# Performance work log

Measured on AMD Instinct MI355X. Metric: run time of the kernel, lower is better.

Reference implementation:

```python
import jax, jax.numpy as jnp
import numpy as np

N = 40000      # nodes
E = 20000      # hyperedges
M = 640000     # incidences
D = 128        # num_features == num_classes == MLP_hidden
ALPHA = 0.1
EPS = 1e-5


def _layernorm(h, g, b):
    mu = jnp.mean(h, axis=-1, keepdims=True)
    var = jnp.mean((h - mu) ** 2, axis=-1, keepdims=True)
    return (h - mu) * jax.lax.rsqrt(var + EPS) * g + b


def _mlp(x, w1, b1, g, be, w2, b2):
    h = x @ w1 + b1
    h = jax.nn.relu(_layernorm(h, g, be))
    return h @ w2 + b2


def _scatter_mean(vals, idx, num_segments):
    s = jax.ops.segment_sum(vals, idx, num_segments=num_segments)
    cnt = jax.ops.segment_sum(jnp.ones((vals.shape[0],), vals.dtype), idx,
                              num_segments=num_segments)
    return s / jnp.maximum(cnt, 1.0)[:, None]


def setup_inputs() -> dict:
    key = jax.random.key(0)
    ks = jax.random.split(key, 16)
    x = jax.random.normal(ks[0], (N, D), dtype=jnp.float32)
    vertex = jax.random.randint(ks[1], (M,), 0, N)
    edges = jax.random.randint(ks[2], (M,), 0, E)
    edge_index = jnp.stack([vertex, edges]).astype(jnp.int64)

    def lin(k, fin, fout):
        s = 1.0 / np.sqrt(fin)
        kw, kb = jax.random.split(k)
        return (jax.random.uniform(kw, (fin, fout), jnp.float32, -s, s),
                jax.random.uniform(kb, (fout,), jnp.float32, -s, s))

    w1_1, b1_1 = lin(ks[3], D, D)
    w1_2, b1_2 = lin(ks[4], D, D)
    w2_1, b2_1 = lin(ks[5], 2 * D, D)
    w2_2, b2_2 = lin(ks[6], D, D)
    g1 = jnp.ones((D,), jnp.float32)
    be1 = jnp.zeros((D,), jnp.float32)
    g2 = jnp.ones((D,), jnp.float32)
    be2 = jnp.zeros((D,), jnp.float32)
    return {"x": x, "w1_1": w1_1, "b1_1": b1_1, "g1": g1, "be1": be1,
            "w1_2": w1_2, "b1_2": b1_2, "w2_1": w2_1, "b2_1": b2_1,
            "g2": g2, "be2": be2, "w2_2": w2_2, "b2_2": b2_2,
            "edge_index": edge_index}


def reference(x, w1_1, b1_1, g1, be1, w1_2, b1_2,
              w2_1, b2_1, g2, be2, w2_2, b2_2, edge_index):
    vertex = edge_index[0]
    edges = edge_index[1]
    X0 = x
    # gather -> MLP1 -> scatter-mean onto hyperedges
    Xve = _mlp(x[vertex], w1_1, b1_1, g1, be1, w1_2, b1_2)   # [M, D]
    Xe = _scatter_mean(Xve, edges, E)                         # [E, D]
    # gather back -> concat -> MLP2 -> scatter-mean onto nodes
    Xev = Xe[edges]                                           # [M, D]
    Xev = _mlp(jnp.concatenate([x[vertex], Xev], axis=-1),
               w2_1, b2_1, g2, be2, w2_2, b2_2)               # [M, D]
    Xv = _scatter_mean(Xev, vertex, N)                        # [N, D]
    return (1.0 - ALPHA) * Xv + ALPHA * X0
```

## Files before the change

### kernel.cpp

```cpp
#include <hip/hip_runtime.h>

#define DF 128
constexpr int NN = 40000;
constexpr int EE = 20000;
constexpr int MM = 640000;
constexpr float EPSF = 1e-5f;
constexpr float ALPHA = 0.1f;
constexpr int SE = 88;
constexpr int SV = 56;

constexpr int NB_BUILD = MM / 256;
constexpr int NB_GEMM  = (NN + 63) / 64;
constexpr int NB_COMBO = (128 * 128 + 128 + 255) / 256;

template <int EPI, bool STATS>
__device__ __forceinline__ void gemm_tile(const float* __restrict__ A, int nrows,
                                          const float* __restrict__ W,
                                          const float* __restrict__ bias,
                                          const float* __restrict__ bias2,
                                          const int* __restrict__ cnt,
                                          const float* __restrict__ g,
                                          const float* __restrict__ be,
                                          const float* __restrict__ xres,
                                          float* __restrict__ C,
                                          float* __restrict__ sOut,
                                          float* __restrict__ qOut,
                                          int blk, float* as) {
  int tid = threadIdx.x;
  int rbase = blk * 64;

  #pragma unroll
  for (int j = 0; j < 8; ++j) {
    int q = tid + j * 256;
    int row = q >> 5;
    int c4 = q & 31;
    int grow = rbase + row;
    float4 v = make_float4(0.f, 0.f, 0.f, 0.f);
    if (grow < nrows) {
      v = *reinterpret_cast<const float4*>(A + (size_t)grow * DF + c4 * 4);
    }
    *reinterpret_cast<float4*>(&as[row * 132 + c4 * 4]) = v;
  }
  __syncthreads();

  int tc = tid & 15;
  int tr = tid >> 4;
  int cbase = tc * 8;

  float acc[4][8];
  #pragma unroll
  for (int i = 0; i < 4; ++i)
    #pragma unroll
    for (int c = 0; c < 8; ++c) acc[i][c] = 0.0f;

  #pragma unroll 4
  for (int k = 0; k < 128; ++k) {
    float w[8];
    *reinterpret_cast<float4*>(&w[0]) = *reinterpret_cast<const float4*>(W + k * DF + cbase);
    *reinterpret_cast<float4*>(&w[4]) = *reinterpret_cast<const float4*>(W + k * DF + cbase + 4);
    float a[4];
    #pragma unroll
    for (int i = 0; i < 4; ++i) a[i] = as[(tr * 4 + i) * 132 + k];
    #pragma unroll
    for (int i = 0; i < 4; ++i)
      #pragma unroll
      for (int c = 0; c < 8; ++c) acc[i][c] += a[i] * w[c];
  }

  float bv[8];
  #pragma unroll
  for (int c = 0; c < 8; ++c) bv[c] = 0.0f;
  if (bias) {
    #pragma unroll
    for (int c = 0; c < 8; ++c) bv[c] = bias[cbase + c];
  }
  if (bias2) {
    #pragma unroll
    for (int c = 0; c < 8; ++c) bv[c] += bias2[cbase + c];
  }
  #pragma unroll
  for (int i = 0; i < 4; ++i)
    #pragma unroll
    for (int c = 0; c < 8; ++c) acc[i][c] += bv[c];

  if (STATS) {
    #pragma unroll
    for (int i = 0; i < 4; ++i) {
      float s = 0.f, q = 0.f;
      #pragma unroll
      for (int c = 0; c < 8; ++c) { s += acc[i][c]; q += acc[i][c] * acc[i][c]; }
      #pragma unroll
      for (int mask = 1; mask <= 8; mask <<= 1) {
        s += __shfl_xor(s, mask, 16);
        q += __shfl_xor(q, mask, 16);
      }
      if (tc == 0) {
        int grow = rbase + tr * 4 + i;
        if (grow < nrows) { sOut[grow] = s; qOut[grow] = q; }
      }
    }
  }

  if (EPI == 1) {
    float gv[8], bev[8];
    #pragma unroll
    for (int c = 0; c < 8; ++c) { gv[c] = g[cbase + c]; bev[c] = be[cbase + c]; }
    #pragma unroll
    for (int i = 0; i < 4; ++i) {
      float s = 0.f, s2 = 0.f;
      #pragma unroll
      for (int c = 0; c < 8; ++c) { s += acc[i][c]; s2 += acc[i][c] * acc[i][c]; }
      #pragma unroll
      for (int mask = 1; mask <= 8; mask <<= 1) {
        s += __shfl_xor(s, mask, 16);
        s2 += __shfl_xor(s2, mask, 16);
      }
      float mean = s * (1.0f / 128.0f);
      float var = s2 * (1.0f / 128.0f) - mean * mean;
      float rs = rsqrtf(var + EPSF);
      #pragma unroll
      for (int c = 0; c < 8; ++c) {
        float y = (acc[i][c] - mean) * rs * gv[c] + bev[c];
        acc[i][c] = fmaxf(y, 0.0f);
      }
    }
  }

  #pragma unroll
  for (int i = 0; i < 4; ++i) {
    int grow = rbase + tr * 4 + i;
    if (grow >= nrows) continue;
    float outv[8];
    if (EPI == 2) {
      int cv = cnt[grow];
      #pragma unroll
      for (int c = 0; c < 8; ++c) {
        float xv = xres[(size_t)grow * DF + cbase + c];
        outv[c] = (cv == 0) ? ALPHA * xv : (1.0f - ALPHA) * acc[i][c] + ALPHA * xv;
      }
    } else {
      #pragma unroll
      for (int c = 0; c < 8; ++c) outv[c] = acc[i][c];
    }
    *reinterpret_cast<float4*>(C + (size_t)grow * DF + cbase) =
        make_float4(outv[0], outv[1], outv[2], outv[3]);
    *reinterpret_cast<float4*>(C + (size_t)grow * DF + cbase + 4) =
        make_float4(outv[4], outv[5], outv[6], outv[7]);
  }
}

__global__ __launch_bounds__(256) void fusedA(
    const int* __restrict__ ei,
    int* __restrict__ cnt_e, int* __restrict__ cnt_v,
    ushort* __restrict__ lst_e, ushort* __restrict__ lst_v,
    const float* __restrict__ x,
    const float* __restrict__ w1_1, const float* __restrict__ b1_1,
    const float* __restrict__ g1, const float* __restrict__ be1,
    const float* __restrict__ w2_1,
    const float* __restrict__ w1_2, const float* __restrict__ b1_2,
    float* __restrict__ H1, float* __restrict__ A2,
    float* __restrict__ sA, float* __restrict__ qA,
    float* __restrict__ Wc, float* __restrict__ bc) {
  __shared__ float as[64 * 132];
  int blk = blockIdx.x;
  if (blk < NB_BUILD) {
    int m = blk * 256 + threadIdx.x;
    int v = ei[m];
    int e = ei[MM + m];
    int pe = atomicAdd(&cnt_e[e], 1);
    lst_e[e * SE + pe] = (ushort)v;
    int pv = atomicAdd(&cnt_v[v], 1);
    lst_v[v * SV + pv] = (ushort)e;
  } else if (blk < NB_BUILD + NB_GEMM) {
    gemm_tile<1, false>(x, NN, w1_1, b1_1, nullptr, nullptr, g1, be1, nullptr,
                        H1, nullptr, nullptr, blk - NB_BUILD, as);
  } else if (blk < NB_BUILD + 2 * NB_GEMM) {
    gemm_tile<0, true>(x, NN, w2_1, nullptr, nullptr, nullptr, nullptr, nullptr,
                       nullptr, A2, sA, qA, blk - NB_BUILD - NB_GEMM, as);
  } else {
    const float* w2b = w2_1 + 128 * DF;
    int out = (blk - NB_BUILD - 2 * NB_GEMM) * 256 + threadIdx.x;
    if (out < 16384) {
      int i = out >> 7;
      int j = out & 127;
      float s = 0.0f;
      for (int k = 0; k < 128; ++k) s += w1_2[i * DF + k] * w2b[k * DF + j];
      Wc[out] = s;
    } else if (out < 16512) {
      int j = out - 16384;
      float s = 0.0f;
      for (int k = 0; k < 128; ++k) s += b1_2[k] * w2b[k * DF + j];
      bc[j] = s;
    }
  }
}

template <int EPI, bool STATS>
__global__ __launch_bounds__(256) void gemm128(const float* __restrict__ A, int nrows,
                                               const float* __restrict__ W,
                                               const float* __restrict__ bias,
                                               const float* __restrict__ bias2,
                                               const int* __restrict__ cnt,
                                               const float* __restrict__ g,
                                               const float* __restrict__ be,
                                               const float* __restrict__ xres,
                                               float* __restrict__ C,
                                               float* __restrict__ sOut,
                                               float* __restrict__ qOut) {
  __shared__ float as[64 * 132];
  gemm_tile<EPI, STATS>(A, nrows, W, bias, bias2, cnt, g, be, xres, C, sOut,
                        qOut, blockIdx.x, as);
}

__global__ __launch_bounds__(256) void gather1(const float* __restrict__ H1,
                                               const int* __restrict__ cnt_e,
                                               const ushort* __restrict__ lst_e,
                                               float* __restrict__ Hemean) {
  int e = blockIdx.x * 4 + (threadIdx.x >> 6);
  int lane = threadIdx.x & 63;
  int g = lane >> 4;
  int l = lane & 15;
  int deg = cnt_e[e];
  const ushort* lst = lst_e + e * SE;
  float4 acc0 = make_float4(0.f, 0.f, 0.f, 0.f);
  float4 acc1 = make_float4(0.f, 0.f, 0.f, 0.f);
  for (int i = g; i < deg; i += 4) {
    int v = lst[i];
    const float* src = H1 + (size_t)v * DF + l * 8;
    float4 h0 = *reinterpret_cast<const float4*>(src);
    float4 h1 = *reinterpret_cast<const float4*>(src + 4);
    acc0.x += h0.x; acc0.y += h0.y; acc0.z += h0.z; acc0.w += h0.w;
    acc1.x += h1.x; acc1.y += h1.y; acc1.z += h1.z; acc1.w += h1.w;
  }
  #pragma unroll
  for (int mask = 16; mask <= 32; mask <<= 1) {
    acc0.x += __shfl_xor(acc0.x, mask); acc0.y += __shfl_xor(acc0.y, mask);
    acc0.z += __shfl_xor(acc0.z, mask); acc0.w += __shfl_xor(acc0.w, mask);
    acc1.x += __shfl_xor(acc1.x, mask); acc1.y += __shfl_xor(acc1.y, mask);
    acc1.z += __shfl_xor(acc1.z, mask); acc1.w += __shfl_xor(acc1.w, mask);
  }
  if (g == 0) {
    float sc = 1.0f / (float)(deg > 1 ? deg : 1);
    float* dst = Hemean + (size_t)e * DF + l * 8;
    *reinterpret_cast<float4*>(dst) =
        make_float4(acc0.x * sc, acc0.y * sc, acc0.z * sc, acc0.w * sc);
    *reinterpret_cast<float4*>(dst + 4) =
        make_float4(acc1.x * sc, acc1.y * sc, acc1.z * sc, acc1.w * sc);
  }
}

__global__ __launch_bounds__(256) void gather2(const float* __restrict__ A2,
                                               const float* __restrict__ B,
                                               const float* __restrict__ sA,
                                               const float* __restrict__ qA,
                                               const float* __restrict__ sB,
                                               const float* __restrict__ qB,
                                               const int* __restrict__ cnt_v,
                                               const ushort* __restrict__ lst_v,
                                               const float* __restrict__ g2,
                                               const float* __restrict__ be2,
                                               float* __restrict__ Svmean) {
  int v = blockIdx.x * 4 + (threadIdx.x >> 6);
  int lane = threadIdx.x & 63;
  int g = lane >> 4;
  int l = lane & 15;
  const float* ap = A2 + (size_t)v * DF + l * 8;
  float4 a0 = *reinterpret_cast<const float4*>(ap);
  float4 a1 = *reinterpret_cast<const float4*>(ap + 4);
  float4 gv0 = *reinterpret_cast<const float4*>(g2 + l * 8);
  float4 gv1 = *reinterpret_cast<const float4*>(g2 + l * 8 + 4);
  float4 bv0 = *reinterpret_cast<const float4*>(be2 + l * 8);
  float4 bv1 = *reinterpret_cast<const float4*>(be2 + l * 8 + 4);
  float sAv = sA[v];
  float qAv = qA[v];
  int deg = cnt_v[v];
  const ushort* lst = lst_v + v * SV;
  float4 acc0 = make_float4(0.f, 0.f, 0.f, 0.f);
  float4 acc1 = make_float4(0.f, 0.f, 0.f, 0.f);
  for (int i = g; i < deg; i += 4) {
    int e = lst[i];
    const float* bp = B + (size_t)e * DF + l * 8;
    float4 b0 = *reinterpret_cast<const float4*>(bp);
    float4 b1 = *reinterpret_cast<const float4*>(bp + 4);
    float d = a0.x * b0.x + a0.y * b0.y + a0.z * b0.z + a0.w * b0.w +
              a1.x * b1.x + a1.y * b1.y + a1.z * b1.z + a1.w * b1.w;
    d += __shfl_xor(d, 1, 16);
    d += __shfl_xor(d, 2, 16);
    d += __shfl_xor(d, 4, 16);
    d += __shfl_xor(d, 8, 16);
    float s = sAv + sB[e];
    float q = qAv + qB[e] + 2.0f * d;
    float mean = s * (1.0f / 128.0f);
    float var = q * (1.0f / 128.0f) - mean * mean;
    float rs = rsqrtf(var + EPSF);
    float mrs = mean * rs;
    float t;
    t = (a0.x + b0.x) * rs - mrs; acc0.x += fmaxf(t * gv0.x + bv0.x, 0.f);
    t = (a0.y + b0.y) * rs - mrs; acc0.y += fmaxf(t * gv0.y + bv0.y, 0.f);
    t = (a0.z + b0.z) * rs - mrs; acc0.z += fmaxf(t * gv0.z + bv0.z, 0.f);
    t = (a0.w + b0.w) * rs - mrs; acc0.w += fmaxf(t * gv0.w + bv0.w, 0.f);
    t = (a1.x + b1.x) * rs - mrs; acc1.x += fmaxf(t * gv1.x + bv1.x, 0.f);
    t = (a1.y + b1.y) * rs - mrs; acc1.y += fmaxf(t * gv1.y + bv1.y, 0.f);
    t = (a1.z + b1.z) * rs - mrs; acc1.z += fmaxf(t * gv1.z + bv1.z, 0.f);
    t = (a1.w + b1.w) * rs - mrs; acc1.w += fmaxf(t * gv1.w + bv1.w, 0.f);
  }
  #pragma unroll
  for (int mask = 16; mask <= 32; mask <<= 1) {
    acc0.x += __shfl_xor(acc0.x, mask); acc0.y += __shfl_xor(acc0.y, mask);
    acc0.z += __shfl_xor(acc0.z, mask); acc0.w += __shfl_xor(acc0.w, mask);
    acc1.x += __shfl_xor(acc1.x, mask); acc1.y += __shfl_xor(acc1.y, mask);
    acc1.z += __shfl_xor(acc1.z, mask); acc1.w += __shfl_xor(acc1.w, mask);
  }
  if (g == 0) {
    float sc = 1.0f / (float)(deg > 1 ? deg : 1);
    float* dst = Svmean + (size_t)v * DF + l * 8;
    *reinterpret_cast<float4*>(dst) =
        make_float4(acc0.x * sc, acc0.y * sc, acc0.z * sc, acc0.w * sc);
    *reinterpret_cast<float4*>(dst + 4) =
        make_float4(acc1.x * sc, acc1.y * sc, acc1.z * sc, acc1.w * sc);
  }
}

extern "C" void kernel_launch(void* const* d_in, const int* in_sizes, int n_in,
                              void* d_out, int out_size, void* d_ws, size_t ws_size,
                              hipStream_t stream) {
  const float* x    = (const float*)d_in[0];
  const float* w1_1 = (const float*)d_in[1];
  const float* b1_1 = (const float*)d_in[2];
  const float* g1   = (const float*)d_in[3];
  const float* be1  = (const float*)d_in[4];
  const float* w1_2 = (const float*)d_in[5];
  const float* b1_2 = (const float*)d_in[6];
  const float* w2_1 = (const float*)d_in[7];
  const float* b2_1 = (const float*)d_in[8];
  const float* g2   = (const float*)d_in[9];
  const float* be2  = (const float*)d_in[10];
  const float* w2_2 = (const float*)d_in[11];
  const float* b2_2 = (const float*)d_in[12];
  const int* ei     = (const int*)d_in[13];
  float* out = (float*)d_out;

  float* ws = (float*)d_ws;
  float* bufN1 = ws;
  float* bufN2 = ws + 5120000;
  float* bufE  = ws + 10240000;
  float* Wc    = ws + 12800000;
  float* bc    = ws + 12816384;
  float* sA    = ws + 12816512;
  float* qA    = ws + 12856512;
  float* sB    = ws + 12896512;
  float* qB    = ws + 12916512;
  int*   ints  = (int*)(ws + 12936512);
  int* cnt_e  = ints;
  int* cnt_v  = ints + 20000;
  ushort* lst_e = (ushort*)(ints + 60000);
  ushort* lst_v = (ushort*)(ints + 60000 + 880000);

  hipMemsetAsync(cnt_e, 0, 60000 * sizeof(int), stream);

  fusedA<<<NB_BUILD + 2 * NB_GEMM + NB_COMBO, 256, 0, stream>>>(
      ei, cnt_e, cnt_v, lst_e, lst_v, x, w1_1, b1_1, g1, be1, w2_1, w1_2, b1_2,
      bufN1, bufN2, sA, qA, Wc, bc);

  gather1<<<EE / 4, 256, 0, stream>>>(bufN1, cnt_e, lst_e, bufE);

  gemm128<0, true><<<(EE + 63) / 64, 256, 0, stream>>>(
      bufE, EE, Wc, bc, b2_1, nullptr, nullptr, nullptr, nullptr, bufE, sB, qB);

  gather2<<<NN / 4, 256, 0, stream>>>(bufN2, bufE, sA, qA, sB, qB,
                                      cnt_v, lst_v, g2, be2, bufN1);

  gemm128<2, false><<<(NN + 63) / 64, 256, 0, stream>>>(
      bufN1, NN, w2_2, b2_2, nullptr, cnt_v, nullptr, nullptr, x, out,
      nullptr, nullptr);
}
```

Measured before the change: 387.1 us.

## Partition adjacency-build atomics by block-id role for XCD-local counters

The incidence-list build is moved after the GEMM blocks in the fused kernel and restructured. Every build block now scans 1024 incidences but only handles ids whose low 3 bits match blockIdx&7. Counters are re-laid out so that each of those 8 residue classes is contiguous, and per-node/edge list strides are padded to 96/64. The intent is to keep each atomic counter touched by blocks that run on the same XCD, which should cut cross-die atomic contention and coherence traffic. The cost is that the edge_index array is read 8 times over and the list buffers grow, which uses more workspace.

```diff
diff --git a/kernel.cpp b/kernel.cpp
--- a/kernel.cpp
+++ b/kernel.cpp
@@ -6,12 +6,17 @@
 constexpr int MM = 640000;
 constexpr float EPSF = 1e-5f;
 constexpr float ALPHA = 0.1f;
-constexpr int SE = 88;
-constexpr int SV = 56;
-
-constexpr int NB_BUILD = MM / 256;
-constexpr int NB_GEMM  = (NN + 63) / 64;
-constexpr int NB_COMBO = (128 * 128 + 128 + 255) / 256;
+constexpr int SE = 96;
+constexpr int SV = 64;
+
+constexpr int NB_G1 = (NN + 63) / 64;
+constexpr int NB_G2 = (NN + 63) / 64;
+constexpr int NB_CB = (128 * 128 + 128 + 255) / 256;
+constexpr int NB_GEMMS = NB_G1 + NB_G2 + NB_CB;
+constexpr int NB_BUILD = 5000;
+
+__device__ __forceinline__ int cidxE(int e) { return (e & 7) * (EE >> 3) + (e >> 3); }
+__device__ __forceinline__ int cidxV(int v) { return (v & 7) * (NN >> 3) + (v >> 3); }
 
 template <int EPI, bool STATS>
 __device__ __forceinline__ void gemm_tile(const float* __restrict__ A, int nrows,
@@ -132,7 +137,7 @@
     if (grow >= nrows) continue;
     float outv[8];
     if (EPI == 2) {
-      int cv = cnt[grow];
+      int cv = cnt[(grow & 7) * (NN >> 3) + (grow >> 3)];
       #pragma unroll
       for (int c = 0; c < 8; ++c) {
         float xv = xres[(size_t)grow * DF + cbase + c];
@@ -163,23 +168,15 @@
     float* __restrict__ Wc, float* __restrict__ bc) {
   __shared__ float as[64 * 132];
   int blk = blockIdx.x;
-  if (blk < NB_BUILD) {
-    int m = blk * 256 + threadIdx.x;
-    int v = ei[m];
-    int e = ei[MM + m];
-    int pe = atomicAdd(&cnt_e[e], 1);
-    lst_e[e * SE + pe] = (ushort)v;
-    int pv = atomicAdd(&cnt_v[v], 1);
-    lst_v[v * SV + pv] = (ushort)e;
-  } else if (blk < NB_BUILD + NB_GEMM) {
+  if (blk < NB_G1) {
     gemm_tile<1, false>(x, NN, w1_1, b1_1, nullptr, nullptr, g1, be1, nullptr,
-                        H1, nullptr, nullptr, blk - NB_BUILD, as);
-  } else if (blk < NB_BUILD + 2 * NB_GEMM) {
+                        H1, nullptr, nullptr, blk, as);
+  } else if (blk < NB_G1 + NB_G2) {
     gemm_tile<0, true>(x, NN, w2_1, nullptr, nullptr, nullptr, nullptr, nullptr,
-                       nullptr, A2, sA, qA, blk - NB_BUILD - NB_GEMM, as);
-  } else {
+                       nullptr, A2, sA, qA, blk - NB_G1, as);
+  } else if (blk < NB_GEMMS) {
     const float* w2b = w2_1 + 128 * DF;
-    int out = (blk - NB_BUILD - 2 * NB_GEMM) * 256 + threadIdx.x;
+    int out = (blk - NB_G1 - NB_G2) * 256 + threadIdx.x;
     if (out < 16384) {
       int i = out >> 7;
       int j = out & 127;
@@ -191,6 +188,24 @@
       float s = 0.0f;
       for (int k = 0; k < 128; ++k) s += b1_2[k] * w2b[k * DF + j];
       bc[j] = s;
+    }
+  } else {
+    int b = blk - NB_GEMMS;
+    int role = blk & 7;
+    int group = b >> 3;
+    #pragma unroll
+    for (int k = 0; k < 4; ++k) {
+      int m = (group * 4 + k) * 256 + threadIdx.x;
+      int v = ei[m];
+      int e = ei[MM + m];
+      if ((e & 7) == role) {
+        int pe = atomicAdd(&cnt_e[role * (EE >> 3) + (e >> 3)], 1);
+        lst_e[e * SE + pe] = (ushort)v;
+      }
+      if ((v & 7) == role) {
+        int pv = atomicAdd(&cnt_v[role * (NN >> 3) + (v >> 3)], 1);
+        lst_v[v * SV + pv] = (ushort)e;
+      }
     }
   }
 }
@@ -220,7 +235,7 @@
   int lane = threadIdx.x & 63;
   int g = lane >> 4;
   int l = lane & 15;
-  int deg = cnt_e[e];
+  int deg = cnt_e[cidxE(e)];
   const ushort* lst = lst_e + e * SE;
   float4 acc0 = make_float4(0.f, 0.f, 0.f, 0.f);
   float4 acc1 = make_float4(0.f, 0.f, 0.f, 0.f);
@@ -273,7 +288,7 @@
   float4 bv1 = *reinterpret_cast<const float4*>(be2 + l * 8 + 4);
   float sAv = sA[v];
   float qAv = qA[v];
-  int deg = cnt_v[v];
+  int deg = cnt_v[cidxV(v)];
   const ushort* lst = lst_v + v * SV;
   float4 acc0 = make_float4(0.f, 0.f, 0.f, 0.f);
   float4 acc1 = make_float4(0.f, 0.f, 0.f, 0.f);
@@ -354,11 +369,11 @@
   int* cnt_e  = ints;
   int* cnt_v  = ints + 20000;
   ushort* lst_e = (ushort*)(ints + 60000);
-  ushort* lst_v = (ushort*)(ints + 60000 + 880000);
+  ushort* lst_v = (ushort*)(ints + 60000 + 960000);
 
   hipMemsetAsync(cnt_e, 0, 60000 * sizeof(int), stream);
 
-  fusedA<<<NB_BUILD + 2 * NB_GEMM + NB_COMBO, 256, 0, stream>>>(
+  fusedA<<<NB_GEMMS + NB_BUILD, 256, 0, stream>>>(
       ei, cnt_e, cnt_v, lst_e, lst_v, x, w1_1, b1_1, g1, be1, w2_1, w1_2, b1_2,
       bufN1, bufN2, sA, qA, Wc, bc);
 
```

Measured after the change: 331.4 us. 14.4% less time.
